# Kernel tuning notes

Measured on AMD Instinct MI355X. Metric: run time of the kernel, lower is better.

## Reference

```python
import jax, jax.numpy as jnp
import numpy as np

N_QUBITS = 4
DIM = 2 ** N_QUBITS  # 16
BATCH = 2 ** 21


def setup_inputs() -> dict:
    key = jax.random.key(0)
    k1, k2 = jax.random.split(key)
    x = jax.random.normal(k1, (BATCH, DIM), dtype=jnp.float32)
    q_weights = jax.random.normal(k2, (N_QUBITS,), dtype=jnp.float32)
    return {"x": x, "q_weights": q_weights}


def _pauli_z_signs():
    # wire 0 is the most-significant bit in default.qubit's amplitude ordering
    idx = jnp.arange(DIM)
    cols = [1.0 - 2.0 * ((idx >> (N_QUBITS - 1 - i)) & 1) for i in range(N_QUBITS)]
    return jnp.stack(cols, axis=1).astype(jnp.float32)  # [16, 4]


def reference(x, q_weights):
    # NaN scrub + reshape, as in the original call()
    x = jnp.where(jnp.isnan(x), jnp.zeros_like(x), x).reshape(-1, DIM)
    # AmplitudeEmbedding(normalize=True): per-sample L2 normalization
    norm = jnp.sqrt(jnp.sum(x * x, axis=1, keepdims=True))
    state = (x / norm).astype(jnp.complex64)
    B = state.shape[0]
    state = state.reshape((B,) + (2,) * N_QUBITS)  # [B,2,2,2,2]
    half = q_weights.astype(jnp.float32) * 0.5
    c, s = jnp.cos(half), jnp.sin(half)
    # RX(theta) = [[cos(t/2), -i sin(t/2)], [-i sin(t/2), cos(t/2)]], applied per wire
    for i in range(N_QUBITS):
        U = jnp.stack([
            jnp.stack([c[i] + 0j, -1j * s[i]]),
            jnp.stack([-1j * s[i], c[i] + 0j]),
        ]).astype(jnp.complex64)  # [2,2]
        axis = 1 + i
        state = jnp.moveaxis(jnp.tensordot(state, U, axes=[[axis], [1]]), -1, axis)
    probs = (state.real ** 2 + state.imag ** 2).reshape(B, DIM)  # [B,16]
    # <Z_i> = sum_k p_k * (+1 if bit_i(k)==0 else -1)
    return probs @ _pauli_z_signs()  # [B, n_qubits]
```

## Files before the change

kernel.cpp:

```cpp
#include <hip/hip_runtime.h>


constexpr int BLOCK = 256;
constexpr int MAX_BLOCKS = 2048;

typedef float fvec4 __attribute__((ext_vector_type(4)));

__global__ __launch_bounds__(BLOCK) void quantum_z_kernel(
    const float* __restrict__ x,
    const float* __restrict__ w,
    float* __restrict__ out,
    int n_vec4)
{
    const int j0 = threadIdx.x & 3;
    const float cw = cosf(w[j0]);

    const int stride = gridDim.x * BLOCK;
    for (int gid = blockIdx.x * BLOCK + threadIdx.x; gid < n_vec4; gid += stride) {
        int j = gid & 3;

        fvec4 v = reinterpret_cast<const fvec4*>(x)[gid];

        float a = (v.x != v.x) ? 0.0f : v.x;
        float b = (v.y != v.y) ? 0.0f : v.y;
        float c = (v.z != v.z) ? 0.0f : v.z;
        float d = (v.w != v.w) ? 0.0f : v.w;

        float p0 = a * a, p1 = b * b, p2 = c * c, p3 = d * d;
        float q  = (p0 + p1) + (p2 + p3);
        float t2 = p2 + p3;
        float t3 = p1 + p3;

        float r1   = __shfl_xor(q, 1);
        float pair = q + r1;
        float oddq = (j & 1) ? q : r1;
        float r2   = __shfl_xor(pair, 2);
        float SS   = pair + r2;
        float S0   = (j & 2) ? pair : r2;
        float S1   = oddq + __shfl_xor(oddq, 2);
        float S2   = t2 + __shfl_xor(t2, 1);
        S2 += __shfl_xor(S2, 2);
        float S3   = t3 + __shfl_xor(t3, 1);
        S3 += __shfl_xor(S3, 2);

        float Sj = (j & 2) ? ((j & 1) ? S3 : S2) : ((j & 1) ? S1 : S0);
        float z  = cw * (1.0f - 2.0f * Sj / SS);
        __builtin_nontemporal_store(z, out + gid);
    }
}

extern "C" void kernel_launch(void* const* d_in, const int* in_sizes, int n_in,
                              void* d_out, int out_size, void* d_ws, size_t ws_size,
                              hipStream_t stream) {
    const float* x = (const float*)d_in[0];
    const float* w = (const float*)d_in[1];
    float* out = (float*)d_out;

    int n_vec4 = in_sizes[0] / 4;
    int grid = (n_vec4 + BLOCK - 1) / BLOCK;
    if (grid > MAX_BLOCKS) grid = MAX_BLOCKS;
    hipLaunchKernelGGL(quantum_z_kernel, dim3(grid), dim3(BLOCK), 0, stream,
                       x, w, out, n_vec4);
}
```

Measured before the change: 197.0 us.

## Drop grid-stride loop, use DPP quad permutes and nontemporal loads

Replaces the grid-stride loop with one thread per vec4 and removes the block cap, so each thread does a single load and store. Lane shuffles within a quad become DPP quad_perm moves, which avoids ds_bpermute traffic. Input loads are marked nontemporal, and the final divide is folded into an FMA with a reciprocal-style expression. The cost is more blocks to launch and cosf being evaluated once per thread instead of once per looping thread.

```diff
diff --git a/kernel.cpp b/kernel.cpp
--- a/kernel.cpp
+++ b/kernel.cpp
@@ -2,9 +2,17 @@
 
 
 constexpr int BLOCK = 256;
-constexpr int MAX_BLOCKS = 2048;
 
 typedef float fvec4 __attribute__((ext_vector_type(4)));
+
+template <int CTRL>
+__device__ __forceinline__ float dpp_qperm(float x) {
+    int r = __builtin_amdgcn_update_dpp(
+        0, __builtin_bit_cast(int, x), CTRL, 0xf, 0xf, true);
+    return __builtin_bit_cast(float, r);
+}
+#define DPP_XOR1 0xB1
+#define DPP_XOR2 0x4E
 
 __global__ __launch_bounds__(BLOCK) void quantum_z_kernel(
     const float* __restrict__ x,
@@ -12,41 +20,38 @@
     float* __restrict__ out,
     int n_vec4)
 {
-    const int j0 = threadIdx.x & 3;
-    const float cw = cosf(w[j0]);
+    int gid = blockIdx.x * BLOCK + threadIdx.x;
+    if (gid >= n_vec4) return;
+    const int j = gid & 3;
+    const float cw = cosf(w[j]);
 
-    const int stride = gridDim.x * BLOCK;
-    for (int gid = blockIdx.x * BLOCK + threadIdx.x; gid < n_vec4; gid += stride) {
-        int j = gid & 3;
+    fvec4 v = __builtin_nontemporal_load(reinterpret_cast<const fvec4*>(x) + gid);
 
-        fvec4 v = reinterpret_cast<const fvec4*>(x)[gid];
+    float a = (v.x != v.x) ? 0.0f : v.x;
+    float b = (v.y != v.y) ? 0.0f : v.y;
+    float c = (v.z != v.z) ? 0.0f : v.z;
+    float d = (v.w != v.w) ? 0.0f : v.w;
 
-        float a = (v.x != v.x) ? 0.0f : v.x;
-        float b = (v.y != v.y) ? 0.0f : v.y;
-        float c = (v.z != v.z) ? 0.0f : v.z;
-        float d = (v.w != v.w) ? 0.0f : v.w;
+    float p0 = a * a, p1 = b * b, p2 = c * c, p3 = d * d;
+    float t2 = p2 + p3;
+    float t3 = p1 + p3;
+    float q  = (p0 + p1) + t2;
 
-        float p0 = a * a, p1 = b * b, p2 = c * c, p3 = d * d;
-        float q  = (p0 + p1) + (p2 + p3);
-        float t2 = p2 + p3;
-        float t3 = p1 + p3;
+    float r1q  = dpp_qperm<DPP_XOR1>(q);
+    float pair = q + r1q;
+    float oddq = (j & 1) ? q : r1q;
+    float r2p  = dpp_qperm<DPP_XOR2>(pair);
+    float SS   = pair + r2p;
+    float S0   = (j & 2) ? pair : r2p;
+    float S1   = oddq + dpp_qperm<DPP_XOR2>(oddq);
+    float S2   = t2 + dpp_qperm<DPP_XOR1>(t2);
+    S2 += dpp_qperm<DPP_XOR2>(S2);
+    float S3   = t3 + dpp_qperm<DPP_XOR1>(t3);
+    S3 += dpp_qperm<DPP_XOR2>(S3);
 
-        float r1   = __shfl_xor(q, 1);
-        float pair = q + r1;
-        float oddq = (j & 1) ? q : r1;
-        float r2   = __shfl_xor(pair, 2);
-        float SS   = pair + r2;
-        float S0   = (j & 2) ? pair : r2;
-        float S1   = oddq + __shfl_xor(oddq, 2);
-        float S2   = t2 + __shfl_xor(t2, 1);
-        S2 += __shfl_xor(S2, 2);
-        float S3   = t3 + __shfl_xor(t3, 1);
-        S3 += __shfl_xor(S3, 2);
-
-        float Sj = (j & 2) ? ((j & 1) ? S3 : S2) : ((j & 1) ? S1 : S0);
-        float z  = cw * (1.0f - 2.0f * Sj / SS);
-        __builtin_nontemporal_store(z, out + gid);
-    }
+    float Sj = (j & 2) ? ((j & 1) ? S3 : S2) : ((j & 1) ? S1 : S0);
+    float z  = cw * __builtin_fmaf(Sj, -2.0f / SS, 1.0f);
+    __builtin_nontemporal_store(z, out + gid);
 }
 
 extern "C" void kernel_launch(void* const* d_in, const int* in_sizes, int n_in,
@@ -58,7 +63,6 @@
 
     int n_vec4 = in_sizes[0] / 4;
     int grid = (n_vec4 + BLOCK - 1) / BLOCK;
-    if (grid > MAX_BLOCKS) grid = MAX_BLOCKS;
     hipLaunchKernelGGL(quantum_z_kernel, dim3(grid), dim3(BLOCK), 0, stream,
                        x, w, out, n_vec4);
 }
```

Measured after the change: 196.3 us. Within noise of the previous version (-0.3%).
